# Optimization experiments

Hardware: AMD Instinct MI355X
Metric: run time of the kernel (lower is better)

The kernel has to match this reference:

```python
import jax, jax.numpy as jnp
import numpy as np

C = 8.0  # RG-LRU temporal-gate constant (Griffin paper, c = 8)


def setup_inputs() -> dict:
    key = jax.random.key(0)
    ks = jax.random.split(key, 4)
    S, B, D = 2048, 8, 2048  # (seq_len, batch, width); batch_first=False layout
    s = 1.0 / np.sqrt(D).astype(np.float32)
    return {
        "x": jax.random.normal(ks[0], (S, B, D), jnp.float32),
        "h0": jnp.zeros((B, D), jnp.float32),
        "W_x": jax.random.normal(ks[1], (D, D), jnp.float32) * s,
        "b_x": jnp.zeros((D,), jnp.float32),
        "W_a": jax.random.normal(ks[2], (D, D), jnp.float32) * s,
        "b_a": jnp.zeros((D,), jnp.float32),
        "a_param": jax.random.uniform(ks[3], (D,), jnp.float32, 0.3, 1.0),
    }


def _rg_lru(x, h0, W_x, b_x, W_a, b_a, a_param):
    # x: (S, B, D) time-major. RG-LRU (Griffin/Hawk), num_heads=1 so the
    # block-diagonal gate projections are plain dense D->D linears.
    S = x.shape[0]
    gate_x = jax.nn.sigmoid(jnp.einsum("sbd,ed->sbe", x, W_x) + b_x)  # input gate
    gate_a = jax.nn.sigmoid(jnp.einsum("sbd,ed->sbe", x, W_a) + b_a)  # recurrence gate
    log_a = -C * gate_a * jax.nn.softplus(a_param)  # (S, B, D), log of decay in (0,1)
    a = jnp.exp(log_a)
    multiplier = jnp.sqrt(1.0 - jnp.exp(2.0 * log_a))  # sqrt(1 - a^2) normalizer
    # Reset at segment start (t == 0): multiplier -> 1, decay -> 0 (cache cleared).
    reset = (jnp.arange(S) == 0)[:, None, None]
    multiplier = jnp.where(reset, 1.0, multiplier)
    a = jnp.where(reset, 0.0, a)
    normed_x = x * gate_x * multiplier  # gated, variance-normalized input

    def step(h, inp):
        a_t, x_t = inp
        h = a_t * h + x_t  # diagonal linear recurrence
        return h, h

    hn, y = jax.lax.scan(step, h0, (a, normed_x))
    return y, hn  # y: (S, B, D) since batch_first=False; hn: (B, D)


def reference(x, h0, W_x, b_x, W_a, b_a, a_param):
    return _rg_lru(x, h0, W_x, b_x, W_a, b_a, a_param)
```

## Files before the change

### kernel.cpp

```cpp
#include <hip/hip_runtime.h>
#include <cstdint>

#define S_LEN 2048
#define B_SZ 8
#define D_DIM 2048
#define M_DIM (S_LEN * B_SZ)
#define CHAINS (B_SZ * D_DIM)
#define BK 64
#define KTILES (D_DIM / BK)

typedef __bf16 bf16;
typedef bf16 bf16x8 __attribute__((ext_vector_type(8)));
typedef bf16 bf16x4 __attribute__((ext_vector_type(4)));
typedef float f32x4 __attribute__((ext_vector_type(4)));

__device__ __forceinline__ void async_copy16(void* lds, const void* g) {
    __builtin_amdgcn_global_load_lds(
        (const __attribute__((address_space(1))) unsigned int*)g,
        (__attribute__((address_space(3))) unsigned int*)lds,
        16, 0, 0);
}

__global__ void k_convert(const float4* __restrict__ x,
                          const float4* __restrict__ wx,
                          const float4* __restrict__ wa,
                          bf16* __restrict__ xb,
                          bf16* __restrict__ wxb,
                          bf16* __restrict__ wab) {
    const long NX4 = (long)M_DIM * D_DIM / 4;
    const long NW4 = (long)D_DIM * D_DIM / 4;
    const long total = NX4 + 2 * NW4;
    for (long i = (long)blockIdx.x * blockDim.x + threadIdx.x; i < total;
         i += (long)gridDim.x * blockDim.x) {
        const float4* s; bf16* d; long k;
        if (i < NX4)            { s = x;  d = xb;  k = i; }
        else if (i < NX4 + NW4) { s = wx; d = wxb; k = i - NX4; }
        else                    { s = wa; d = wab; k = i - NX4 - NW4; }
        float4 v = s[k];
        bf16x4 o;
        o[0] = (bf16)v.x; o[1] = (bf16)v.y; o[2] = (bf16)v.z; o[3] = (bf16)v.w;
        *reinterpret_cast<bf16x4*>(d + 4 * k) = o;
    }
}

__global__ void k_cvec(const float* __restrict__ ap, float* __restrict__ cv) {
    int e = blockIdx.x * blockDim.x + threadIdx.x;
    if (e < D_DIM) {
        float v = ap[e];
        cv[e] = -8.0f * log1pf(expf(v));
    }
}

__global__ __launch_bounds__(256, 2) void k_gemm(
    const bf16* __restrict__ xb,
    const bf16* __restrict__ wxb,
    const bf16* __restrict__ wab,
    const float* __restrict__ x32,
    const float* __restrict__ bx,
    const float* __restrict__ ba,
    const float* __restrict__ cv,
    float* __restrict__ abuf,
    float* __restrict__ y)
{
    __shared__ __align__(16) char smem[48 * 1024];
    char* sA  = smem;
    char* sBx = smem + 16384;
    char* sBa = smem + 32768;

    const int tid  = threadIdx.x;
    const int lane = tid & 63;
    const int w    = tid >> 6;
    const int wr   = w >> 1;
    const int wc   = w & 1;
    const int m0 = blockIdx.y * 128;
    const int e0 = blockIdx.x * 128;

    f32x4 accx[4][4];
    f32x4 acca[4][4];
#pragma unroll
    for (int i = 0; i < 4; ++i)
#pragma unroll
        for (int j = 0; j < 4; ++j) {
            accx[i][j] = (f32x4)(0.0f);
            acca[i][j] = (f32x4)(0.0f);
        }

    const int srow   = lane >> 3;
    const int schunk = lane & 7;

    for (int kt = 0; kt < KTILES; ++kt) {
        const long kcolb = (long)kt * (BK * 2);

#pragma unroll
        for (int j = 0; j < 4; ++j) {
            const int baseRow = (w * 4 + j) * 8;
            const int row = baseRow + srow;
            const int swz = schunk ^ (row & 7);
            const long rowbyA = (long)(m0 + row) * (D_DIM * 2) + kcolb + swz * 16;
            async_copy16(sA + baseRow * 128, (const char*)xb + rowbyA);
            const long rowbyB = (long)(e0 + row) * (D_DIM * 2) + kcolb + swz * 16;
            async_copy16(sBx + baseRow * 128, (const char*)wxb + rowbyB);
            async_copy16(sBa + baseRow * 128, (const char*)wab + rowbyB);
        }
        __syncthreads();

#pragma unroll
        for (int ks = 0; ks < 2; ++ks) {
            const int kchunk = ks * 4 + (lane >> 4);
            bf16x8 af[4], bxf[4], baf[4];
#pragma unroll
            for (int i = 0; i < 4; ++i) {
                const int r = wr * 64 + i * 16 + (lane & 15);
                const int pc = kchunk ^ (r & 7);
                af[i] = *reinterpret_cast<const bf16x8*>(sA + r * 128 + pc * 16);
            }
#pragma unroll
            for (int j = 0; j < 4; ++j) {
                const int r = wc * 64 + j * 16 + (lane & 15);
                const int pc = kchunk ^ (r & 7);
                bxf[j] = *reinterpret_cast<const bf16x8*>(sBx + r * 128 + pc * 16);
                baf[j] = *reinterpret_cast<const bf16x8*>(sBa + r * 128 + pc * 16);
            }
#pragma unroll
            for (int i = 0; i < 4; ++i)
#pragma unroll
                for (int j = 0; j < 4; ++j) {
                    accx[i][j] = __builtin_amdgcn_mfma_f32_16x16x32_bf16(
                        af[i], bxf[j], accx[i][j], 0, 0, 0);
                    acca[i][j] = __builtin_amdgcn_mfma_f32_16x16x32_bf16(
                        af[i], baf[j], acca[i][j], 0, 0, 0);
                }
        }
        __syncthreads();
    }

    const int colL = lane & 15;
    const int rgrp = lane >> 4;
#pragma unroll
    for (int j = 0; j < 4; ++j) {
        const int e = e0 + wc * 64 + j * 16 + colL;
        const float bxv = bx[e];
        const float bav = ba[e];
        const float cvv = cv[e];
#pragma unroll
        for (int i = 0; i < 4; ++i) {
            const int mbase = m0 + wr * 64 + i * 16 + rgrp * 4;
#pragma unroll
            for (int r = 0; r < 4; ++r) {
                const int m = mbase + r;
                const float zx = accx[i][j][r] + bxv;
                const float za = acca[i][j][r] + bav;
                const float gx = 1.0f / (1.0f + __expf(-zx));
                const float ga = 1.0f / (1.0f + __expf(-za));
                const float la = cvv * ga;
                float a = __expf(la);
                float mult = sqrtf(fmaxf(1.0f - a * a, 0.0f));
                if (m < B_SZ) { a = 0.0f; mult = 1.0f; }
                const long o = (long)m * D_DIM + e;
                const float xv = x32[o];
                abuf[o] = a;
                y[o] = xv * gx * mult;
            }
        }
    }
}

__global__ __launch_bounds__(64) void k_scan(
    const float* __restrict__ abuf,
    float* __restrict__ y,
    const float* __restrict__ h0,
    float* __restrict__ hn) {
    const int c = blockIdx.x * 64 + threadIdx.x;
    float h = h0[c];

    float av0[16], xv0[16], av1[16], xv1[16];
#pragma unroll
    for (int j = 0; j < 16; ++j) {
        const long o = (long)j * CHAINS + c;
        av0[j] = abuf[o];
        xv0[j] = y[o];
    }
    for (int g = 0; g < 128; g += 2) {
        const long base1 = ((long)(g + 1) * 16) * CHAINS + c;
        if (g + 1 < 128) {
#pragma unroll
            for (int j = 0; j < 16; ++j) {
                av1[j] = abuf[base1 + (long)j * CHAINS];
                xv1[j] = y[base1 + (long)j * CHAINS];
            }
        }
        const long base0 = ((long)g * 16) * CHAINS + c;
#pragma unroll
        for (int j = 0; j < 16; ++j) {
            h = fmaf(av0[j], h, xv0[j]);
            y[base0 + (long)j * CHAINS] = h;
        }
        const long base2 = ((long)(g + 2) * 16) * CHAINS + c;
        if (g + 2 < 128) {
#pragma unroll
            for (int j = 0; j < 16; ++j) {
                av0[j] = abuf[base2 + (long)j * CHAINS];
                xv0[j] = y[base2 + (long)j * CHAINS];
            }
        }
        if (g + 1 < 128) {
#pragma unroll
            for (int j = 0; j < 16; ++j) {
                h = fmaf(av1[j], h, xv1[j]);
                y[base1 + (long)j * CHAINS] = h;
            }
        }
    }
    hn[c] = h;
}

extern "C" void kernel_launch(void* const* d_in, const int* in_sizes, int n_in,
                              void* d_out, int out_size, void* d_ws, size_t ws_size,
                              hipStream_t stream) {
    const float* x  = (const float*)d_in[0];
    const float* h0 = (const float*)d_in[1];
    const float* Wx = (const float*)d_in[2];
    const float* bx = (const float*)d_in[3];
    const float* Wa = (const float*)d_in[4];
    const float* ba = (const float*)d_in[5];
    const float* ap = (const float*)d_in[6];
    float* out = (float*)d_out;

    char* ws = (char*)d_ws;
    bf16*  xb   = (bf16*)(ws);
    bf16*  wxb  = (bf16*)(ws + 67108864L);
    bf16*  wab  = (bf16*)(ws + 75497472L);
    float* cv   = (float*)(ws + 83886080L);
    float* abuf = (float*)(ws + 83894272L);

    float* y  = out;
    float* hn = out + (long)M_DIM * D_DIM;

    k_convert<<<dim3(2048), dim3(256), 0, stream>>>(
        (const float4*)x, (const float4*)Wx, (const float4*)Wa, xb, wxb, wab);
    k_cvec<<<dim3(8), dim3(256), 0, stream>>>(ap, cv);
    k_gemm<<<dim3(D_DIM / 128, M_DIM / 128), dim3(256), 0, stream>>>(
        xb, wxb, wab, x, bx, ba, cv, abuf, y);
    k_scan<<<dim3(CHAINS / 64), dim3(64), 0, stream>>>(abuf, y, h0, hn);
}
```

Measured before the change: 506.2 us.

## Double-buffer GEMM tiles with 8-wave 256x128 blocks and phased MFMA/prefetch

The fused dual GEMM moves from 4-wave 128x128 tiles to 8-wave 256x128 tiles with 128KB of double-buffered LDS. Loads for the next k-tile are spread across four compute phases, and each phase is bracketed by barriers and s_setprio. A 1D grid with an XCD-aware block remap replaces the 2D grid. The goal is to hide global-to-LDS latency behind MFMA work and improve cache reuse, at the cost of higher LDS use (one block per CU) and more barriers.

```diff
diff --git a/kernel.cpp b/kernel.cpp
--- a/kernel.cpp
+++ b/kernel.cpp
@@ -51,7 +51,7 @@
     }
 }
 
-__global__ __launch_bounds__(256, 2) void k_gemm(
+__global__ __launch_bounds__(512, 2) void k_gemm(
     const bf16* __restrict__ xb,
     const bf16* __restrict__ wxb,
     const bf16* __restrict__ wab,
@@ -62,18 +62,62 @@
     float* __restrict__ abuf,
     float* __restrict__ y)
 {
-    __shared__ __align__(16) char smem[48 * 1024];
-    char* sA  = smem;
-    char* sBx = smem + 16384;
-    char* sBa = smem + 32768;
+    __shared__ __align__(16) char smem[131072];
 
     const int tid  = threadIdx.x;
     const int lane = tid & 63;
     const int w    = tid >> 6;
-    const int wr   = w >> 1;
-    const int wc   = w & 1;
-    const int m0 = blockIdx.y * 128;
-    const int e0 = blockIdx.x * 128;
+    const int wm   = w >> 1;
+    const int wn   = w & 1;
+
+    const int orig = blockIdx.x;
+    const int wgid = (orig & 7) * 128 + (orig >> 3);
+    const int m0 = (wgid >> 4) * 256;
+    const int e0 = (wgid & 15) * 128;
+
+    const int srow  = lane >> 3;
+    const int swz16 = ((lane & 7) ^ srow) * 16;
+
+    const char* gA  = (const char*)xb;
+    const char* gBx = (const char*)wxb;
+    const char* gBa = (const char*)wab;
+
+#define STAGE_A(buf, kt, p) do {                                               \
+    const long kb_ = (long)(kt) * 128 + swz16;                                 \
+    _Pragma("unroll")                                                          \
+    for (int j_ = 0; j_ < 2; ++j_) {                                           \
+        const int br_ = w * 32 + ((p) * 2 + j_) * 8;                           \
+        async_copy16(smem + (buf) * 65536 + br_ * 128,                         \
+                     gA + ((long)(m0 + br_ + srow) * 4096 + kb_));             \
+    } } while (0)
+
+#define STAGE_BX(buf, kt) do {                                                 \
+    const long kb_ = (long)(kt) * 128 + swz16;                                 \
+    _Pragma("unroll")                                                          \
+    for (int j_ = 0; j_ < 2; ++j_) {                                           \
+        const int br_ = w * 16 + j_ * 8;                                       \
+        async_copy16(smem + (buf) * 65536 + 32768 + br_ * 128,                 \
+                     gBx + ((long)(e0 + br_ + srow) * 4096 + kb_));            \
+    } } while (0)
+
+#define STAGE_BA(buf, kt) do {                                                 \
+    const long kb_ = (long)(kt) * 128 + swz16;                                 \
+    _Pragma("unroll")                                                          \
+    for (int j_ = 0; j_ < 2; ++j_) {                                           \
+        const int br_ = w * 16 + j_ * 8;                                       \
+        async_copy16(smem + (buf) * 65536 + 49152 + br_ * 128,                 \
+                     gBa + ((long)(e0 + br_ + srow) * 4096 + kb_));            \
+    } } while (0)
+
+#define PHASE_MID() do {                                                       \
+    __builtin_amdgcn_s_barrier();                                              \
+    asm volatile("s_waitcnt lgkmcnt(0)" ::: "memory");                         \
+    __builtin_amdgcn_sched_barrier(0);                                         \
+    __builtin_amdgcn_s_setprio(1); } while (0)
+
+#define PHASE_END() do {                                                       \
+    __builtin_amdgcn_s_setprio(0);                                             \
+    __builtin_amdgcn_s_barrier(); } while (0)
 
     f32x4 accx[4][4];
     f32x4 acca[4][4];
@@ -85,66 +129,113 @@
             acca[i][j] = (f32x4)(0.0f);
         }
 
-    const int srow   = lane >> 3;
-    const int schunk = lane & 7;
+    STAGE_A(0, 0, 0); STAGE_A(0, 0, 1); STAGE_BX(0, 0); STAGE_BA(0, 0);
+    asm volatile("s_waitcnt vmcnt(0)" ::: "memory");
+    __builtin_amdgcn_s_barrier();
+
+    const int rL  = lane & 15;
+    const int ch0 = ((0 + (lane >> 4)) ^ (lane & 7)) * 16;
+    const int ch1 = ((4 + (lane >> 4)) ^ (lane & 7)) * 16;
 
     for (int kt = 0; kt < KTILES; ++kt) {
-        const long kcolb = (long)kt * (BK * 2);
-
-#pragma unroll
-        for (int j = 0; j < 4; ++j) {
-            const int baseRow = (w * 4 + j) * 8;
-            const int row = baseRow + srow;
-            const int swz = schunk ^ (row & 7);
-            const long rowbyA = (long)(m0 + row) * (D_DIM * 2) + kcolb + swz * 16;
-            async_copy16(sA + baseRow * 128, (const char*)xb + rowbyA);
-            const long rowbyB = (long)(e0 + row) * (D_DIM * 2) + kcolb + swz * 16;
-            async_copy16(sBx + baseRow * 128, (const char*)wxb + rowbyB);
-            async_copy16(sBa + baseRow * 128, (const char*)wab + rowbyB);
-        }
-        __syncthreads();
-
-#pragma unroll
-        for (int ks = 0; ks < 2; ++ks) {
-            const int kchunk = ks * 4 + (lane >> 4);
-            bf16x8 af[4], bxf[4], baf[4];
-#pragma unroll
-            for (int i = 0; i < 4; ++i) {
-                const int r = wr * 64 + i * 16 + (lane & 15);
-                const int pc = kchunk ^ (r & 7);
-                af[i] = *reinterpret_cast<const bf16x8*>(sA + r * 128 + pc * 16);
-            }
-#pragma unroll
-            for (int j = 0; j < 4; ++j) {
-                const int r = wc * 64 + j * 16 + (lane & 15);
-                const int pc = kchunk ^ (r & 7);
-                bxf[j] = *reinterpret_cast<const bf16x8*>(sBx + r * 128 + pc * 16);
-                baf[j] = *reinterpret_cast<const bf16x8*>(sBa + r * 128 + pc * 16);
-            }
-#pragma unroll
-            for (int i = 0; i < 4; ++i)
-#pragma unroll
-                for (int j = 0; j < 4; ++j) {
-                    accx[i][j] = __builtin_amdgcn_mfma_f32_16x16x32_bf16(
-                        af[i], bxf[j], accx[i][j], 0, 0, 0);
-                    acca[i][j] = __builtin_amdgcn_mfma_f32_16x16x32_bf16(
-                        af[i], baf[j], acca[i][j], 0, 0, 0);
-                }
-        }
-        __syncthreads();
-    }
-
-    const int colL = lane & 15;
+        const int c  = kt & 1;
+        const int nb = 1 - c;
+        char* sA  = smem + c * 65536;
+        char* sBx = sA + 32768;
+        char* sBa = sA + 49152;
+        const bool pf = (kt < KTILES - 1);
+
+        bf16x8 af[4], bf[4];
+
+#pragma unroll
+        for (int i = 0; i < 4; ++i) {
+            const int r = wm * 64 + i * 16 + rL;
+            af[i] = *reinterpret_cast<const bf16x8*>(sA + r * 128 + ch0);
+        }
+#pragma unroll
+        for (int j = 0; j < 4; ++j) {
+            const int r = wn * 64 + j * 16 + rL;
+            bf[j] = *reinterpret_cast<const bf16x8*>(sBx + r * 128 + ch0);
+        }
+        if (pf) STAGE_A(nb, kt + 1, 0);
+        PHASE_MID();
+#pragma unroll
+        for (int i = 0; i < 4; ++i)
+#pragma unroll
+            for (int j = 0; j < 4; ++j)
+                accx[i][j] = __builtin_amdgcn_mfma_f32_16x16x32_bf16(
+                    af[i], bf[j], accx[i][j], 0, 0, 0);
+        PHASE_END();
+
+#pragma unroll
+        for (int j = 0; j < 4; ++j) {
+            const int r = wn * 64 + j * 16 + rL;
+            bf[j] = *reinterpret_cast<const bf16x8*>(sBa + r * 128 + ch0);
+        }
+        if (pf) STAGE_A(nb, kt + 1, 1);
+        PHASE_MID();
+#pragma unroll
+        for (int i = 0; i < 4; ++i)
+#pragma unroll
+            for (int j = 0; j < 4; ++j)
+                acca[i][j] = __builtin_amdgcn_mfma_f32_16x16x32_bf16(
+                    af[i], bf[j], acca[i][j], 0, 0, 0);
+        PHASE_END();
+
+#pragma unroll
+        for (int i = 0; i < 4; ++i) {
+            const int r = wm * 64 + i * 16 + rL;
+            af[i] = *reinterpret_cast<const bf16x8*>(sA + r * 128 + ch1);
+        }
+#pragma unroll
+        for (int j = 0; j < 4; ++j) {
+            const int r = wn * 64 + j * 16 + rL;
+            bf[j] = *reinterpret_cast<const bf16x8*>(sBx + r * 128 + ch1);
+        }
+        if (pf) STAGE_BX(nb, kt + 1);
+        PHASE_MID();
+#pragma unroll
+        for (int i = 0; i < 4; ++i)
+#pragma unroll
+            for (int j = 0; j < 4; ++j)
+                accx[i][j] = __builtin_amdgcn_mfma_f32_16x16x32_bf16(
+                    af[i], bf[j], accx[i][j], 0, 0, 0);
+        PHASE_END();
+
+#pragma unroll
+        for (int j = 0; j < 4; ++j) {
+            const int r = wn * 64 + j * 16 + rL;
+            bf[j] = *reinterpret_cast<const bf16x8*>(sBa + r * 128 + ch1);
+        }
+        if (pf) STAGE_BA(nb, kt + 1);
+        PHASE_MID();
+#pragma unroll
+        for (int i = 0; i < 4; ++i)
+#pragma unroll
+            for (int j = 0; j < 4; ++j)
+                acca[i][j] = __builtin_amdgcn_mfma_f32_16x16x32_bf16(
+                    af[i], bf[j], acca[i][j], 0, 0, 0);
+        __builtin_amdgcn_s_setprio(0);
+        if (pf) asm volatile("s_waitcnt vmcnt(0)" ::: "memory");
+        __builtin_amdgcn_s_barrier();
+    }
+
+#undef STAGE_A
+#undef STAGE_BX
+#undef STAGE_BA
+#undef PHASE_MID
+#undef PHASE_END
+
     const int rgrp = lane >> 4;
 #pragma unroll
     for (int j = 0; j < 4; ++j) {
-        const int e = e0 + wc * 64 + j * 16 + colL;
+        const int e = e0 + wn * 64 + j * 16 + rL;
         const float bxv = bx[e];
         const float bav = ba[e];
         const float cvv = cv[e];
 #pragma unroll
         for (int i = 0; i < 4; ++i) {
-            const int mbase = m0 + wr * 64 + i * 16 + rgrp * 4;
+            const int mbase = m0 + wm * 64 + i * 16 + rgrp * 4;
 #pragma unroll
             for (int r = 0; r < 4; ++r) {
                 const int m = mbase + r;
@@ -239,7 +330,7 @@
     k_convert<<<dim3(2048), dim3(256), 0, stream>>>(
         (const float4*)x, (const float4*)Wx, (const float4*)Wa, xb, wxb, wab);
     k_cvec<<<dim3(8), dim3(256), 0, stream>>>(ap, cv);
-    k_gemm<<<dim3(D_DIM / 128, M_DIM / 128), dim3(256), 0, stream>>>(
+    k_gemm<<<dim3(M_DIM / 256 * (D_DIM / 128)), dim3(512), 0, stream>>>(
         xb, wxb, wab, x, bx, ba, cv, abuf, y);
     k_scan<<<dim3(CHAINS / 64), dim3(64), 0, stream>>>(abuf, y, h0, hn);
 }
```

Measured after the change: 486.2 us. 1.04x faster.

## Split GEMM tile by gate across waves and remap blocks for XCD locality

Applied to the files above, without the earlier changes.

The fused dual-gate GEMM changes from 128x128 tiles, where each wave computed both gates, to 128x64 tiles where half the waves compute the x-gate and half the a-gate. This halves accumulator registers per wave so occupancy can rise to three blocks per CU. The a-gate results are then exchanged through LDS for the epilogue, and block IDs are remapped so neighbouring tiles land on the same XCD. In exchange, the A tile is reloaded for twice as many blocks, and the epilogue adds an LDS round trip and runs on only half the waves.

```diff
diff --git a/kernel.cpp b/kernel.cpp
--- a/kernel.cpp
+++ b/kernel.cpp
@@ -51,7 +51,7 @@
     }
 }
 
-__global__ __launch_bounds__(256, 2) void k_gemm(
+__global__ __launch_bounds__(256, 3) void k_gemm(
     const bf16* __restrict__ xb,
     const bf16* __restrict__ wxb,
     const bf16* __restrict__ wab,
@@ -62,104 +62,121 @@
     float* __restrict__ abuf,
     float* __restrict__ y)
 {
-    __shared__ __align__(16) char smem[48 * 1024];
-    char* sA  = smem;
-    char* sBx = smem + 16384;
-    char* sBa = smem + 32768;
+    __shared__ __align__(16) char smem[34816];
 
     const int tid  = threadIdx.x;
     const int lane = tid & 63;
     const int w    = tid >> 6;
-    const int wr   = w >> 1;
-    const int wc   = w & 1;
-    const int m0 = blockIdx.y * 128;
-    const int e0 = blockIdx.x * 128;
-
-    f32x4 accx[4][4];
-    f32x4 acca[4][4];
+    const int gate = w >> 1;
+    const int wm   = w & 1;
+
+    const int orig = blockIdx.x;
+    const int wgid = (orig & 7) * 512 + (orig >> 3);
+    const int m0 = (wgid & 127) * 128;
+    const int e0 = (wgid >> 7) * 64;
+
+    char* sA  = smem;
+    char* sBx = smem + 16384;
+    char* sBa = smem + 24576;
+    char* sB  = gate ? sBa : sBx;
+
+    const int srow  = lane >> 3;
+    const int swz16 = ((lane & 7) ^ srow) * 16;
+
+    const char* gA  = (const char*)xb;
+    const char* gBx = (const char*)wxb;
+    const char* gBa = (const char*)wab;
+
+    f32x4 acc[4][4];
 #pragma unroll
     for (int i = 0; i < 4; ++i)
 #pragma unroll
+        for (int j = 0; j < 4; ++j) acc[i][j] = (f32x4)(0.0f);
+
+    const int rL = lane & 15;
+
+    for (int kt = 0; kt < KTILES; ++kt) {
+        const long kb = (long)kt * 128 + swz16;
+
+#pragma unroll
+        for (int jj = 0; jj < 4; ++jj) {
+            const int br = w * 32 + jj * 8;
+            async_copy16(sA + br * 128, gA + ((long)(m0 + br + srow) * 4096 + kb));
+        }
+#pragma unroll
+        for (int jj = 0; jj < 2; ++jj) {
+            const int br = w * 16 + jj * 8;
+            async_copy16(sBx + br * 128, gBx + ((long)(e0 + br + srow) * 4096 + kb));
+            async_copy16(sBa + br * 128, gBa + ((long)(e0 + br + srow) * 4096 + kb));
+        }
+        __syncthreads();
+
+#pragma unroll
+        for (int ks = 0; ks < 2; ++ks) {
+            const int ch = ((ks * 4 + (lane >> 4)) ^ (lane & 7)) * 16;
+            bf16x8 af[4], bf[4];
+#pragma unroll
+            for (int i = 0; i < 4; ++i) {
+                const int r = wm * 64 + i * 16 + rL;
+                af[i] = *reinterpret_cast<const bf16x8*>(sA + r * 128 + ch);
+            }
+#pragma unroll
+            for (int j = 0; j < 4; ++j) {
+                const int r = j * 16 + rL;
+                bf[j] = *reinterpret_cast<const bf16x8*>(sB + r * 128 + ch);
+            }
+#pragma unroll
+            for (int i = 0; i < 4; ++i)
+#pragma unroll
+                for (int j = 0; j < 4; ++j)
+                    acc[i][j] = __builtin_amdgcn_mfma_f32_16x16x32_bf16(
+                        af[i], bf[j], acc[i][j], 0, 0, 0);
+        }
+        __syncthreads();
+    }
+
+    float* zl = (float*)smem;
+    const int rgrp = lane >> 4;
+
+    if (gate == 1) {
+#pragma unroll
+        for (int j = 0; j < 4; ++j)
+#pragma unroll
+            for (int i = 0; i < 4; ++i)
+#pragma unroll
+                for (int r = 0; r < 4; ++r) {
+                    const int ml = i * 16 + rgrp * 4 + r;
+                    const int el = j * 16 + rL;
+                    zl[(wm * 64 + ml) * 66 + el] = acc[i][j][r];
+                }
+    }
+    __syncthreads();
+    if (gate == 0) {
+#pragma unroll
         for (int j = 0; j < 4; ++j) {
-            accx[i][j] = (f32x4)(0.0f);
-            acca[i][j] = (f32x4)(0.0f);
-        }
-
-    const int srow   = lane >> 3;
-    const int schunk = lane & 7;
-
-    for (int kt = 0; kt < KTILES; ++kt) {
-        const long kcolb = (long)kt * (BK * 2);
-
-#pragma unroll
-        for (int j = 0; j < 4; ++j) {
-            const int baseRow = (w * 4 + j) * 8;
-            const int row = baseRow + srow;
-            const int swz = schunk ^ (row & 7);
-            const long rowbyA = (long)(m0 + row) * (D_DIM * 2) + kcolb + swz * 16;
-            async_copy16(sA + baseRow * 128, (const char*)xb + rowbyA);
-            const long rowbyB = (long)(e0 + row) * (D_DIM * 2) + kcolb + swz * 16;
-            async_copy16(sBx + baseRow * 128, (const char*)wxb + rowbyB);
-            async_copy16(sBa + baseRow * 128, (const char*)wab + rowbyB);
-        }
-        __syncthreads();
-
-#pragma unroll
-        for (int ks = 0; ks < 2; ++ks) {
-            const int kchunk = ks * 4 + (lane >> 4);
-            bf16x8 af[4], bxf[4], baf[4];
+            const int e = e0 + j * 16 + rL;
+            const float bxv = bx[e];
+            const float bav = ba[e];
+            const float cvv = cv[e];
 #pragma unroll
             for (int i = 0; i < 4; ++i) {
-                const int r = wr * 64 + i * 16 + (lane & 15);
-                const int pc = kchunk ^ (r & 7);
-                af[i] = *reinterpret_cast<const bf16x8*>(sA + r * 128 + pc * 16);
-            }
-#pragma unroll
-            for (int j = 0; j < 4; ++j) {
-                const int r = wc * 64 + j * 16 + (lane & 15);
-                const int pc = kchunk ^ (r & 7);
-                bxf[j] = *reinterpret_cast<const bf16x8*>(sBx + r * 128 + pc * 16);
-                baf[j] = *reinterpret_cast<const bf16x8*>(sBa + r * 128 + pc * 16);
-            }
-#pragma unroll
-            for (int i = 0; i < 4; ++i)
-#pragma unroll
-                for (int j = 0; j < 4; ++j) {
-                    accx[i][j] = __builtin_amdgcn_mfma_f32_16x16x32_bf16(
-                        af[i], bxf[j], accx[i][j], 0, 0, 0);
-                    acca[i][j] = __builtin_amdgcn_mfma_f32_16x16x32_bf16(
-                        af[i], baf[j], acca[i][j], 0, 0, 0);
+#pragma unroll
+                for (int r = 0; r < 4; ++r) {
+                    const int ml = i * 16 + rgrp * 4 + r;
+                    const int m = m0 + wm * 64 + ml;
+                    const float zx = acc[i][j][r] + bxv;
+                    const float za = zl[(wm * 64 + ml) * 66 + j * 16 + rL] + bav;
+                    const float gx = 1.0f / (1.0f + __expf(-zx));
+                    const float ga = 1.0f / (1.0f + __expf(-za));
+                    const float la = cvv * ga;
+                    float a = __expf(la);
+                    float mult = sqrtf(fmaxf(1.0f - a * a, 0.0f));
+                    if (m < B_SZ) { a = 0.0f; mult = 1.0f; }
+                    const long o = (long)m * D_DIM + e;
+                    const float xv = x32[o];
+                    abuf[o] = a;
+                    y[o] = xv * gx * mult;
                 }
-        }
-        __syncthreads();
-    }
-
-    const int colL = lane & 15;
-    const int rgrp = lane >> 4;
-#pragma unroll
-    for (int j = 0; j < 4; ++j) {
-        const int e = e0 + wc * 64 + j * 16 + colL;
-        const float bxv = bx[e];
-        const float bav = ba[e];
-        const float cvv = cv[e];
-#pragma unroll
-        for (int i = 0; i < 4; ++i) {
-            const int mbase = m0 + wr * 64 + i * 16 + rgrp * 4;
-#pragma unroll
-            for (int r = 0; r < 4; ++r) {
-                const int m = mbase + r;
-                const float zx = accx[i][j][r] + bxv;
-                const float za = acca[i][j][r] + bav;
-                const float gx = 1.0f / (1.0f + __expf(-zx));
-                const float ga = 1.0f / (1.0f + __expf(-za));
-                const float la = cvv * ga;
-                float a = __expf(la);
-                float mult = sqrtf(fmaxf(1.0f - a * a, 0.0f));
-                if (m < B_SZ) { a = 0.0f; mult = 1.0f; }
-                const long o = (long)m * D_DIM + e;
-                const float xv = x32[o];
-                abuf[o] = a;
-                y[o] = xv * gx * mult;
             }
         }
     }
@@ -239,7 +256,7 @@
     k_convert<<<dim3(2048), dim3(256), 0, stream>>>(
         (const float4*)x, (const float4*)Wx, (const float4*)Wa, xb, wxb, wab);
     k_cvec<<<dim3(8), dim3(256), 0, stream>>>(ap, cv);
-    k_gemm<<<dim3(D_DIM / 128, M_DIM / 128), dim3(256), 0, stream>>>(
+    k_gemm<<<dim3((M_DIM / 128) * (D_DIM / 64)), dim3(256), 0, stream>>>(
         xb, wxb, wab, x, bx, ba, cv, abuf, y);
     k_scan<<<dim3(CHAINS / 64), dim3(64), 0, stream>>>(abuf, y, h0, hn);
 }
```

Result: slower. 667.1 us (+31.8%).
